# Performance work log

Measured on AMD Instinct MI355X. Metric: run time of the kernel, lower is better.

The kernel has to match this reference:

```python
import jax, jax.numpy as jnp
import numpy as np

T, B, I, H = 512, 512, 128, 512

def setup_inputs() -> dict:
    key = jax.random.key(0)
    ks = jax.random.split(key, 10)
    s = 0.05  # small init scale to avoid gate saturation
    return {
        "x": jax.random.normal(ks[0], (T, B, I), jnp.float32),
        "enc_hiddens": jax.random.normal(ks[1], (1, B, H), jnp.float32),
        "h0": jax.random.normal(ks[2], (1, B, H), jnp.float32) * s,
        "c0": jax.random.normal(ks[3], (1, B, H), jnp.float32) * s,
        "W_ih": jax.random.normal(ks[4], (4 * H, I), jnp.float32) * s,
        "W_hh": jax.random.normal(ks[5], (4 * H, H), jnp.float32) * s,
        "b_ih": jax.random.normal(ks[6], (4 * H,), jnp.float32) * s,
        "b_hh": jax.random.normal(ks[7], (4 * H,), jnp.float32) * s,
        "fc_W": jax.random.normal(ks[8], (I, H), jnp.float32) * s,
        "fc_b": jax.random.normal(ks[9], (I,), jnp.float32) * s,
    }

def reference(x, enc_hiddens, h0, c0, W_ih, W_hh, b_ih, b_hh, fc_W, fc_b):
    # RECURSIVE decoding branch: feed own output back in; store outputs reversed.
    seq_len = x.shape[0]
    b = b_ih + b_hh  # fuse biases

    def step(carry, _):
        inp, h, c = carry  # inp:[B,I], h,c:[B,H]
        gates = inp @ W_ih.T + h @ W_hh.T + b  # [B,4H]
        i_g, f_g, g_g, o_g = jnp.split(gates, 4, axis=-1)  # torch gate order i,f,g,o
        i_g = jax.nn.sigmoid(i_g)
        f_g = jax.nn.sigmoid(f_g)
        g_g = jnp.tanh(g_g)
        o_g = jax.nn.sigmoid(o_g)
        c_new = f_g * c + i_g * g_g
        h_new = o_g * jnp.tanh(c_new)
        out = h_new @ fc_W.T + fc_b            # Linear
        out = 2.0 * jax.nn.sigmoid(out) - 1.0  # use_act affine rescale
        return (out, h_new, c_new), out

    init = (x[seq_len - 1], h0[0], c0[0])
    _, outs = jax.lax.scan(step, init, None, length=seq_len)  # [T,B,I], step t stored at index t
    # original writes dec_outs[seq_len - t - 1], i.e. reversed order
    return jnp.flip(outs, axis=0)
```

## Files before the change

kernel.cpp:

```cpp
#include <hip/hip_runtime.h>

typedef unsigned short u16;
typedef unsigned int   u32;
typedef unsigned long long u64;
typedef short v8s __attribute__((ext_vector_type(8)));
typedef float v16f __attribute__((ext_vector_type(16)));
typedef float v2f  __attribute__((ext_vector_type(2)));

#define B_ 512
#define I_ 128
#define H_ 512
#define KK 640
#define NSTEP 512
#define AST 648

__device__ inline u16 f2b(float x){
  union{float f; unsigned u;} v; v.f = x;
  unsigned r = v.u + 0x7fffu + ((v.u >> 16) & 1u);
  return (u16)(r >> 16);
}

__device__ inline float tanh_fast(float x){
  float e = __expf(2.f * x);
  return 1.f - 2.f / (e + 1.f);
}

__device__ inline u64 ld64(const u16* p){
  return __hip_atomic_load((const u64*)p, __ATOMIC_RELAXED, __HIP_MEMORY_SCOPE_AGENT);
}
__device__ inline void st32(u16* p, u32 v){
  __hip_atomic_store((u32*)p, v, __ATOMIC_RELAXED, __HIP_MEMORY_SCOPE_AGENT);
}
__device__ inline u32 fpoll(const u32* p){
  return __hip_atomic_load(p, __ATOMIC_RELAXED, __HIP_MEMORY_SCOPE_AGENT);
}
__device__ inline void fst(u32* p, u32 v){
  __hip_atomic_store(p, v, __ATOMIC_RELAXED, __HIP_MEMORY_SCOPE_AGENT);
}

__global__ void init_kernel(const float* __restrict__ x, const float* __restrict__ h0,
    const float* __restrict__ Wih, const float* __restrict__ Whh,
    const float* __restrict__ bih, const float* __restrict__ bhh, const float* __restrict__ fcW,
    u16* __restrict__ Wcat, u16* __restrict__ fcWb, float* __restrict__ bsum,
    u16* __restrict__ hb0, u16* __restrict__ outb, u32* __restrict__ flags)
{
  int idx = blockIdx.x * 256 + threadIdx.x;
  if (idx < 1310720) {
    int g = idx / 640, k = idx - g * 640;
    float v = (k < 512) ? Whh[g * 512 + k] : Wih[g * 128 + (k - 512)];
    Wcat[idx] = f2b(v);
  } else if (idx < 1376256) {
    int i = idx - 1310720; fcWb[i] = f2b(fcW[i]);
  } else if (idx < 1378304) {
    int i = idx - 1376256; bsum[i] = bih[i] + bhh[i];
  } else if (idx < 1640448) {
    int i = idx - 1378304; hb0[i] = f2b(h0[i]);
  } else if (idx < 1705984) {
    int i = idx - 1640448; outb[i] = f2b(x[33488896 + i]);
  } else if (idx < 1706240) {
    flags[idx - 1705984] = 0u;
  }
}

__global__ __launch_bounds__(512, 2) void decoder_persist(
    const u16* __restrict__ Wcat, const float* __restrict__ bsum,
    const u16* __restrict__ fcWb, const float* __restrict__ fcb,
    const float* __restrict__ c0,
    u16* __restrict__ hb0, u16* __restrict__ hb1, const u16* __restrict__ outb,
    float* __restrict__ dout, u32* __restrict__ flags)
{
  __shared__ __align__(16) u16  Alds[32 * AST];
  __shared__ __align__(16) float gbuf[4096];

  const int tid  = threadIdx.x;
  const int wid  = tid >> 6, lane = tid & 63;
  const int l31  = lane & 31, q2 = lane >> 5;
  const int mb   = blockIdx.x & 15;
  const int nb   = blockIdx.x >> 4;
  const int R    = mb * 32;
  u32* hf = flags + mb * 16;

  const bool isfc = (wid >= 4);
  const int  wc   = (wid - 4) * 32;

  v8s wfrag[40];
  if (!isfc) {
    const u16* wr = Wcat + (u64)(wid * 512 + nb * 32 + l31) * KK + q2 * 8;
    #pragma unroll
    for (int kc = 0; kc < 40; ++kc) wfrag[kc] = *reinterpret_cast<const v8s*>(wr + kc * 16);
  } else {
    const u16* fr = fcWb + (u64)(wc + l31) * H_ + q2 * 8;
    #pragma unroll
    for (int kc = 0; kc < 32; ++kc) wfrag[kc] = *reinterpret_cast<const v8s*>(fr + kc * 16);
    #pragma unroll
    for (int kc = 32; kc < 40; ++kc) wfrag[kc] = (v8s){0,0,0,0,0,0,0,0};
  }
  const float bias0 = isfc ? fcb[wc + l31] : bsum[wid * 512 + nb * 32 + l31];

  const bool dopred = isfc && (((wc + l31) >> 3) == nb);

  float oreg[16];
  float* dpend = nullptr;

  const int crow = tid >> 4, ccol = (tid * 2) & 31;
  float cv0 = c0[(R + crow) * H_ + nb * 32 + ccol];
  float cv1 = c0[(R + crow) * H_ + nb * 32 + ccol + 1];

  for (int t = 0; t <= NSTEP; ++t) {
    const u16* hsrc = (t & 1) ? hb1 : hb0;

    if (dopred && dpend) {
      #pragma unroll
      for (int r = 0; r < 16; ++r) {
        int row = (r & 3) + 8 * (r >> 2) + 4 * q2;
        __builtin_nontemporal_store(oreg[r], dpend + (R + row) * I_ + wc + l31);
      }
      dpend = nullptr;
    }

    if (t > 0) {
      const u32 tt = (u32)t;
      for (;;) {
        u32 f = fpoll(hf + 2 * wid + (lane & 1));
        if (__all((int)(f >= tt))) break;
      }
      __asm__ volatile("" ::: "memory");
    }

    {
      u64 tmp[8];
      #pragma unroll
      for (int k = 0; k < 8; ++k) {
        int v = k * 64 + lane;
        int row = v >> 4, c16 = v & 15;
        tmp[k] = ld64(hsrc + (R + row) * H_ + wid * 64 + c16 * 4);
      }
      #pragma unroll
      for (int k = 0; k < 8; ++k) {
        int v = k * 64 + lane;
        int row = v >> 4, c16 = v & 15;
        *reinterpret_cast<u64*>(&Alds[row * AST + wid * 64 + c16 * 4]) = tmp[k];
      }
    }
    if (t == 0) {
      u64 tmp[2];
      #pragma unroll
      for (int u = 0; u < 2; ++u) {
        int v = u * 512 + tid;
        int row = v >> 5, cc = v & 31;
        tmp[u] = ld64(outb + (R + row) * I_ + cc * 4);
      }
      #pragma unroll
      for (int u = 0; u < 2; ++u) {
        int v = u * 512 + tid;
        int row = v >> 5, cc = v & 31;
        *reinterpret_cast<u64*>(&Alds[row * AST + 512 + cc * 4]) = tmp[u];
      }
    }
    __syncthreads();

    v16f acc = {0.f,0.f,0.f,0.f,0.f,0.f,0.f,0.f,0.f,0.f,0.f,0.f,0.f,0.f,0.f,0.f};
    const u16* ab = &Alds[l31 * AST + q2 * 8];
    __builtin_amdgcn_s_setprio(1);
    #pragma unroll
    for (int kc = 0; kc < 32; ++kc) {
      v8s a = *reinterpret_cast<const v8s*>(ab + kc * 16);
      acc = __builtin_amdgcn_mfma_f32_32x32x16_bf16(a, wfrag[kc], acc, 0, 0, 0);
    }
    __builtin_amdgcn_s_setprio(0);

    if (isfc && t > 0) {
      #pragma unroll
      for (int r = 0; r < 16; ++r) {
        int row = (r & 3) + 8 * (r >> 2) + 4 * q2;
        float o = 2.f / (1.f + __expf(-(acc[r] + bias0))) - 1.f;
        oreg[r] = o;
        Alds[row * AST + 512 + wc + l31] = f2b(o);
      }
      dpend = dout + (u64)(NSTEP - t) * (B_ * I_);
    }
    __syncthreads();

    if (t < NSTEP) {
      if (!isfc) {
        __builtin_amdgcn_s_setprio(1);
        #pragma unroll
        for (int kc = 32; kc < 40; ++kc) {
          v8s a = *reinterpret_cast<const v8s*>(ab + kc * 16);
          acc = __builtin_amdgcn_mfma_f32_32x32x16_bf16(a, wfrag[kc], acc, 0, 0, 0);
        }
        __builtin_amdgcn_s_setprio(0);
        #pragma unroll
        for (int r = 0; r < 16; ++r) {
          int row = (r & 3) + 8 * (r >> 2) + 4 * q2;
          float z = acc[r] + bias0;
          float a2 = (wid == 2) ? tanh_fast(z) : 1.f / (1.f + __expf(-z));
          gbuf[wid * 1024 + row * 32 + l31] = a2;
        }
      }
      __syncthreads();

      u16* hdst = (t & 1) ? hb0 : hb1;
      v2f ig = *reinterpret_cast<const v2f*>(&gbuf[       crow * 32 + ccol]);
      v2f fg = *reinterpret_cast<const v2f*>(&gbuf[1024 + crow * 32 + ccol]);
      v2f gg = *reinterpret_cast<const v2f*>(&gbuf[2048 + crow * 32 + ccol]);
      v2f og = *reinterpret_cast<const v2f*>(&gbuf[3072 + crow * 32 + ccol]);
      float cn0 = fg[0] * cv0 + ig[0] * gg[0];
      float cn1 = fg[1] * cv1 + ig[1] * gg[1];
      cv0 = cn0; cv1 = cn1;
      u32 packed = (u32)f2b(og[0] * tanh_fast(cn0)) | ((u32)f2b(og[1] * tanh_fast(cn1)) << 16);
      st32(hdst + (R + crow) * H_ + nb * 32 + ccol, packed);
      __syncthreads();
      __asm__ volatile("" ::: "memory");
      if (tid == 0) fst(hf + nb, (u32)(t + 1));
    }
  }

  if (dopred && dpend) {
    #pragma unroll
    for (int r = 0; r < 16; ++r) {
      int row = (r & 3) + 8 * (r >> 2) + 4 * q2;
      __builtin_nontemporal_store(oreg[r], dpend + (R + row) * I_ + wc + l31);
    }
  }
}

extern "C" void kernel_launch(void* const* d_in, const int* in_sizes, int n_in,
                              void* d_out, int out_size, void* d_ws, size_t ws_size,
                              hipStream_t stream)
{
  const float* x   = (const float*)d_in[0];
  const float* h0  = (const float*)d_in[2];
  const float* c0  = (const float*)d_in[3];
  const float* Wih = (const float*)d_in[4];
  const float* Whh = (const float*)d_in[5];
  const float* bih = (const float*)d_in[6];
  const float* bhh = (const float*)d_in[7];
  const float* fcW = (const float*)d_in[8];
  const float* fcb = (const float*)d_in[9];

  char* p = (char*)d_ws;
  u16*   Wcat  = (u16*)p;   p += 2048LL * 640 * 2;
  u16*   fcWb  = (u16*)p;   p += 128 * 512 * 2;
  float* bsum  = (float*)p; p += 2048 * 4;
  u16*   hb0   = (u16*)p;   p += 512 * 512 * 2;
  u16*   hb1   = (u16*)p;   p += 512 * 512 * 2;
  u16*   outb  = (u16*)p;   p += 512 * 128 * 2;
  u32*   flags = (u32*)p;   p += 256 * 4;
  float* dout  = (float*)d_out;

  init_kernel<<<6666, 256, 0, stream>>>(x, h0, Wih, Whh, bih, bhh, fcW,
                                        Wcat, fcWb, bsum, hb0, outb, flags);
  decoder_persist<<<256, 512, 0, stream>>>(Wcat, bsum, fcWb, fcb, c0,
                                           hb0, hb1, outb, dout, flags);
}
```

Baseline: 2.770 ms.

## Interleave gate columns per wave and fuse LSTM cell update with DPP, per-wave flags

Reorders the gate weight columns so that each wave's MFMA tile holds all four gates (i,f,g,o) for 8 hidden units in adjacent lanes. The cell update then runs in registers using DPP quad broadcasts, which removes the shared-memory gate buffer and two block-wide barriers per step. Readiness flags become per-wave instead of per-block, so consumers poll finer-grained flags and producers signal as soon as their own wave finishes. This shortens the recurrent critical path, at the cost of more flag polling, a larger flag array, and a redundant tanh evaluated in all four lanes of each quad.

```diff
diff --git a/kernel.cpp b/kernel.cpp
--- a/kernel.cpp
+++ b/kernel.cpp
@@ -5,7 +5,6 @@
 typedef unsigned long long u64;
 typedef short v8s __attribute__((ext_vector_type(8)));
 typedef float v16f __attribute__((ext_vector_type(16)));
-typedef float v2f  __attribute__((ext_vector_type(2)));
 
 #define B_ 512
 #define I_ 128
@@ -23,6 +22,12 @@
 __device__ inline float tanh_fast(float x){
   float e = __expf(2.f * x);
   return 1.f - 2.f / (e + 1.f);
+}
+
+template<int CTRL>
+__device__ inline float dppf(float x){
+  int i = __builtin_amdgcn_update_dpp(0, __float_as_int(x), CTRL, 0xF, 0xF, true);
+  return __int_as_float(i);
 }
 
 __device__ inline u64 ld64(const u16* p){
@@ -57,7 +62,7 @@
     int i = idx - 1378304; hb0[i] = f2b(h0[i]);
   } else if (idx < 1705984) {
     int i = idx - 1640448; outb[i] = f2b(x[33488896 + i]);
-  } else if (idx < 1706240) {
+  } else if (idx < 1707008) {
     flags[idx - 1705984] = 0u;
   }
 }
@@ -69,8 +74,7 @@
     u16* __restrict__ hb0, u16* __restrict__ hb1, const u16* __restrict__ outb,
     float* __restrict__ dout, u32* __restrict__ flags)
 {
-  __shared__ __align__(16) u16  Alds[32 * AST];
-  __shared__ __align__(16) float gbuf[4096];
+  __shared__ __align__(16) u16 Alds[32 * AST];
 
   const int tid  = threadIdx.x;
   const int wid  = tid >> 6, lane = tid & 63;
@@ -78,14 +82,17 @@
   const int mb   = blockIdx.x & 15;
   const int nb   = blockIdx.x >> 4;
   const int R    = mb * 32;
-  u32* hf = flags + mb * 16;
+  u32* gf = flags + mb * 64;
 
   const bool isfc = (wid >= 4);
   const int  wc   = (wid - 4) * 32;
 
+  const int ggate = l31 & 3, gj = l31 >> 2;
+  const int gcol  = ggate * 512 + nb * 32 + wid * 8 + gj;
+
   v8s wfrag[40];
   if (!isfc) {
-    const u16* wr = Wcat + (u64)(wid * 512 + nb * 32 + l31) * KK + q2 * 8;
+    const u16* wr = Wcat + (u64)gcol * KK + q2 * 8;
     #pragma unroll
     for (int kc = 0; kc < 40; ++kc) wfrag[kc] = *reinterpret_cast<const v8s*>(wr + kc * 16);
   } else {
@@ -95,16 +102,25 @@
     #pragma unroll
     for (int kc = 32; kc < 40; ++kc) wfrag[kc] = (v8s){0,0,0,0,0,0,0,0};
   }
-  const float bias0 = isfc ? fcb[wc + l31] : bsum[wid * 512 + nb * 32 + l31];
+  const float bias0 = isfc ? fcb[wc + l31] : bsum[gcol];
 
   const bool dopred = isfc && (((wc + l31) >> 3) == nb);
 
   float oreg[16];
   float* dpend = nullptr;
 
-  const int crow = tid >> 4, ccol = (tid * 2) & 31;
-  float cv0 = c0[(R + crow) * H_ + nb * 32 + ccol];
-  float cv1 = c0[(R + crow) * H_ + nb * 32 + ccol + 1];
+  float cv[16];
+  if (!isfc) {
+    #pragma unroll
+    for (int r = 0; r < 16; ++r) {
+      int row = (r & 3) + 8 * (r >> 2) + 4 * q2;
+      cv[r] = c0[(R + row) * H_ + nb * 32 + wid * 8 + gj];
+    }
+  }
+
+  const float anum  = (ggate == 2) ? -2.f : 1.f;
+  const float abase = (ggate == 2) ?  1.f : 0.f;
+  const float zmul  = (ggate == 2) ?  2.f : -1.f;
 
   for (int t = 0; t <= NSTEP; ++t) {
     const u16* hsrc = (t & 1) ? hb1 : hb0;
@@ -121,7 +137,7 @@
     if (t > 0) {
       const u32 tt = (u32)t;
       for (;;) {
-        u32 f = fpoll(hf + 2 * wid + (lane & 1));
+        u32 f = fpoll(gf + 8 * wid + (lane & 7));
         if (__all((int)(f >= tt))) break;
       }
       __asm__ volatile("" ::: "memory");
@@ -190,29 +206,30 @@
           acc = __builtin_amdgcn_mfma_f32_32x32x16_bf16(a, wfrag[kc], acc, 0, 0, 0);
         }
         __builtin_amdgcn_s_setprio(0);
+
+        u16* hdst = (t & 1) ? hb0 : hb1;
         #pragma unroll
         for (int r = 0; r < 16; ++r) {
           int row = (r & 3) + 8 * (r >> 2) + 4 * q2;
           float z = acc[r] + bias0;
-          float a2 = (wid == 2) ? tanh_fast(z) : 1.f / (1.f + __expf(-z));
-          gbuf[wid * 1024 + row * 32 + l31] = a2;
+          float e = __expf(zmul * z);
+          float act = abase + anum / (e + 1.f);
+          float ig = dppf<0x00>(act);
+          float fg = dppf<0x55>(act);
+          float gg = dppf<0xAA>(act);
+          float og = dppf<0xFF>(act);
+          float cn = fg * cv[r] + ig * gg;
+          cv[r] = cn;
+          float h = og * tanh_fast(cn);
+          float hn = dppf<0x104>(h);
+          if ((l31 & 7) == 0) {
+            u32 packed = (u32)f2b(h) | ((u32)f2b(hn) << 16);
+            st32(hdst + (R + row) * H_ + nb * 32 + wid * 8 + gj, packed);
+          }
         }
-      }
-      __syncthreads();
-
-      u16* hdst = (t & 1) ? hb0 : hb1;
-      v2f ig = *reinterpret_cast<const v2f*>(&gbuf[       crow * 32 + ccol]);
-      v2f fg = *reinterpret_cast<const v2f*>(&gbuf[1024 + crow * 32 + ccol]);
-      v2f gg = *reinterpret_cast<const v2f*>(&gbuf[2048 + crow * 32 + ccol]);
-      v2f og = *reinterpret_cast<const v2f*>(&gbuf[3072 + crow * 32 + ccol]);
-      float cn0 = fg[0] * cv0 + ig[0] * gg[0];
-      float cn1 = fg[1] * cv1 + ig[1] * gg[1];
-      cv0 = cn0; cv1 = cn1;
-      u32 packed = (u32)f2b(og[0] * tanh_fast(cn0)) | ((u32)f2b(og[1] * tanh_fast(cn1)) << 16);
-      st32(hdst + (R + crow) * H_ + nb * 32 + ccol, packed);
-      __syncthreads();
-      __asm__ volatile("" ::: "memory");
-      if (tid == 0) fst(hf + nb, (u32)(t + 1));
+        __asm__ volatile("s_waitcnt vmcnt(0)" ::: "memory");
+        if (lane == 0) fst(gf + nb * 4 + wid, (u32)(t + 1));
+      }
     }
   }
 
@@ -246,10 +263,10 @@
   u16*   hb0   = (u16*)p;   p += 512 * 512 * 2;
   u16*   hb1   = (u16*)p;   p += 512 * 512 * 2;
   u16*   outb  = (u16*)p;   p += 512 * 128 * 2;
-  u32*   flags = (u32*)p;   p += 256 * 4;
+  u32*   flags = (u32*)p;   p += 1024 * 4;
   float* dout  = (float*)d_out;
 
-  init_kernel<<<6666, 256, 0, stream>>>(x, h0, Wih, Whh, bih, bhh, fcW,
+  init_kernel<<<6672, 256, 0, stream>>>(x, h0, Wih, Whh, bih, bhh, fcW,
                                         Wcat, fcWb, bsum, hb0, outb, flags);
   decoder_persist<<<256, 512, 0, stream>>>(Wcat, bsum, fcWb, fcb, c0,
                                            hb0, hb1, outb, dout, flags);
```

Measured after the change: 5.557 ms. 101% more time.

## Map row-group blocks onto same XCC via hardware ID and use sc0 loads/stores

Applied to the files above, without the earlier changes.

Each block reads its XCC id and claims a (mb, nb) slot through a per-XCC atomic counter, so all 16 blocks sharing a row group and its flags run on the same XCC. The h exchange then uses sc0 global loads and stores, which keeps coherence at XCC L2 scope instead of device scope, with an explicit wait before the flag is published. This targets the per-step cross-XCC synchronisation latency of the persistent LSTM. It assumes exactly 32 blocks land on each of 8 XCCs; if the distribution is uneven, slots wrap and collide, which would give wrong results or a deadlock. The patch also relies on sc0 being enough for visibility within one XCC.

```diff
diff --git a/kernel.cpp b/kernel.cpp
--- a/kernel.cpp
+++ b/kernel.cpp
@@ -27,9 +27,6 @@
 
 __device__ inline u64 ld64(const u16* p){
   return __hip_atomic_load((const u64*)p, __ATOMIC_RELAXED, __HIP_MEMORY_SCOPE_AGENT);
-}
-__device__ inline void st32(u16* p, u32 v){
-  __hip_atomic_store((u32*)p, v, __ATOMIC_RELAXED, __HIP_MEMORY_SCOPE_AGENT);
 }
 __device__ inline u32 fpoll(const u32* p){
   return __hip_atomic_load(p, __ATOMIC_RELAXED, __HIP_MEMORY_SCOPE_AGENT);
@@ -57,7 +54,7 @@
     int i = idx - 1378304; hb0[i] = f2b(h0[i]);
   } else if (idx < 1705984) {
     int i = idx - 1640448; outb[i] = f2b(x[33488896 + i]);
-  } else if (idx < 1706240) {
+  } else if (idx < 1706248) {
     flags[idx - 1705984] = 0u;
   }
 }
@@ -67,18 +64,27 @@
     const u16* __restrict__ fcWb, const float* __restrict__ fcb,
     const float* __restrict__ c0,
     u16* __restrict__ hb0, u16* __restrict__ hb1, const u16* __restrict__ outb,
-    float* __restrict__ dout, u32* __restrict__ flags)
+    float* __restrict__ dout, u32* __restrict__ flags, u32* __restrict__ xcnt)
 {
   __shared__ __align__(16) u16  Alds[32 * AST];
   __shared__ __align__(16) float gbuf[4096];
+  __shared__ u32 claim_sh;
 
   const int tid  = threadIdx.x;
   const int wid  = tid >> 6, lane = tid & 63;
   const int l31  = lane & 31, q2 = lane >> 5;
-  const int mb   = blockIdx.x & 15;
-  const int nb   = blockIdx.x >> 4;
-  const int R    = mb * 32;
-  u32* hf = flags + mb * 16;
+
+  if (tid == 0) {
+    u32 xcc;
+    asm volatile("s_getreg_b32 %0, hwreg(HW_REG_XCC_ID)" : "=s"(xcc));
+    u32 slot = atomicAdd(xcnt + (xcc & 7), 1u);
+    claim_sh = (xcc & 7) * 32 + (slot & 31);
+  }
+  __syncthreads();
+  const int mb = (int)(claim_sh >> 4);
+  const int nb = (int)(claim_sh & 15);
+  const int R  = mb * 32;
+  u32* gf = flags + mb * 16;
 
   const bool isfc = (wid >= 4);
   const int  wc   = (wid - 4) * 32;
@@ -121,26 +127,42 @@
     if (t > 0) {
       const u32 tt = (u32)t;
       for (;;) {
-        u32 f = fpoll(hf + 2 * wid + (lane & 1));
+        u32 f = fpoll(gf + 2 * wid + (lane & 1));
         if (__all((int)(f >= tt))) break;
       }
       __asm__ volatile("" ::: "memory");
     }
 
     {
-      u64 tmp[8];
-      #pragma unroll
-      for (int k = 0; k < 8; ++k) {
-        int v = k * 64 + lane;
-        int row = v >> 4, c16 = v & 15;
-        tmp[k] = ld64(hsrc + (R + row) * H_ + wid * 64 + c16 * 4);
-      }
-      #pragma unroll
-      for (int k = 0; k < 8; ++k) {
-        int v = k * 64 + lane;
-        int row = v >> 4, c16 = v & 15;
-        *reinterpret_cast<u64*>(&Alds[row * AST + wid * 64 + c16 * 4]) = tmp[k];
-      }
+      const int rb = lane >> 4, c16 = lane & 15;
+      const u16* pb = hsrc + (u64)(R + rb) * H_ + wid * 64 + c16 * 4;
+      const u16 *p0 = pb,            *p1 = pb + 4*H_,  *p2 = pb + 8*H_,  *p3 = pb + 12*H_;
+      const u16 *p4 = pb + 16*H_,    *p5 = pb + 20*H_, *p6 = pb + 24*H_, *p7 = pb + 28*H_;
+      u64 t0,t1,t2,t3,t4,t5,t6,t7;
+      asm volatile(
+        "global_load_dwordx2 %[d0], %[a0], off sc0\n\t"
+        "global_load_dwordx2 %[d1], %[a1], off sc0\n\t"
+        "global_load_dwordx2 %[d2], %[a2], off sc0\n\t"
+        "global_load_dwordx2 %[d3], %[a3], off sc0\n\t"
+        "global_load_dwordx2 %[d4], %[a4], off sc0\n\t"
+        "global_load_dwordx2 %[d5], %[a5], off sc0\n\t"
+        "global_load_dwordx2 %[d6], %[a6], off sc0\n\t"
+        "global_load_dwordx2 %[d7], %[a7], off sc0\n\t"
+        "s_waitcnt vmcnt(0)"
+        : [d0]"=&v"(t0),[d1]"=&v"(t1),[d2]"=&v"(t2),[d3]"=&v"(t3),
+          [d4]"=&v"(t4),[d5]"=&v"(t5),[d6]"=&v"(t6),[d7]"=&v"(t7)
+        : [a0]"v"(p0),[a1]"v"(p1),[a2]"v"(p2),[a3]"v"(p3),
+          [a4]"v"(p4),[a5]"v"(p5),[a6]"v"(p6),[a7]"v"(p7)
+        : "memory");
+      u16* lb = &Alds[rb * AST + wid * 64 + c16 * 4];
+      *reinterpret_cast<u64*>(lb              ) = t0;
+      *reinterpret_cast<u64*>(lb +  4 * AST   ) = t1;
+      *reinterpret_cast<u64*>(lb +  8 * AST   ) = t2;
+      *reinterpret_cast<u64*>(lb + 12 * AST   ) = t3;
+      *reinterpret_cast<u64*>(lb + 16 * AST   ) = t4;
+      *reinterpret_cast<u64*>(lb + 20 * AST   ) = t5;
+      *reinterpret_cast<u64*>(lb + 24 * AST   ) = t6;
+      *reinterpret_cast<u64*>(lb + 28 * AST   ) = t7;
     }
     if (t == 0) {
       u64 tmp[2];
@@ -209,10 +231,13 @@
       float cn1 = fg[1] * cv1 + ig[1] * gg[1];
       cv0 = cn0; cv1 = cn1;
       u32 packed = (u32)f2b(og[0] * tanh_fast(cn0)) | ((u32)f2b(og[1] * tanh_fast(cn1)) << 16);
-      st32(hdst + (R + crow) * H_ + nb * 32 + ccol, packed);
+      u16* hp = hdst + (u64)(R + crow) * H_ + nb * 32 + ccol;
+      asm volatile("global_store_dword %[p], %[v], off sc0"
+                   :: [p]"v"(hp), [v]"v"(packed) : "memory");
+      asm volatile("s_waitcnt vmcnt(0)" ::: "memory");
       __syncthreads();
       __asm__ volatile("" ::: "memory");
-      if (tid == 0) fst(hf + nb, (u32)(t + 1));
+      if (tid == 0) fst(gf + nb, (u32)(t + 1));
     }
   }
 
@@ -246,11 +271,12 @@
   u16*   hb0   = (u16*)p;   p += 512 * 512 * 2;
   u16*   hb1   = (u16*)p;   p += 512 * 512 * 2;
   u16*   outb  = (u16*)p;   p += 512 * 128 * 2;
-  u32*   flags = (u32*)p;   p += 256 * 4;
+  u32*   flags = (u32*)p;   p += 512 * 4;
+  u32*   xcnt  = flags + 256;
   float* dout  = (float*)d_out;
 
   init_kernel<<<6666, 256, 0, stream>>>(x, h0, Wih, Whh, bih, bhh, fcW,
                                         Wcat, fcWb, bsum, hb0, outb, flags);
   decoder_persist<<<256, 512, 0, stream>>>(Wcat, bsum, fcWb, fcb, c0,
-                                           hb0, hb1, outb, dout, flags);
-}
+                                           hb0, hb1, outb, dout, flags, xcnt);
+}
```

New measurement: 3.548 ms. 1.28x slower.
